# Optimization experiments

Hardware: AMD Instinct MI355X
Metric: run time of the kernel (lower is better)

## Reference

```python
import jax, jax.numpy as jnp
import numpy as np

B, D, H, E = 1024, 64, 128, 8192


def setup_inputs() -> dict:
    key = jax.random.key(0)
    ks = jax.random.split(key, 10)
    def w(k, shape, fan_in):
        return jax.random.normal(k, shape, jnp.float32) / np.float32(np.sqrt(fan_in))
    return {
        "mu": jax.random.normal(ks[0], (B, D), jnp.float32),
        "current_edge_index": jax.random.randint(ks[1], (2, E), 0, B),
        "W1": w(ks[2], (D, H), D),   "b1": jnp.zeros((H,), jnp.float32),
        "W2": w(ks[3], (H, H), H),   "b2": jnp.zeros((H,), jnp.float32),
        "Ws1": w(ks[4], (2 * H, H), 2 * H), "bs1": jnp.zeros((H,), jnp.float32),
        "Ws2": w(ks[5], (H, 1), H),  "bs2": jnp.zeros((1,), jnp.float32),
        "Wg1": w(ks[6], (2 * H, H), 2 * H), "bg1": jnp.zeros((H,), jnp.float32),
        "Wg2": w(ks[7], (H, D), H), "bg2": jnp.zeros((D,), jnp.float32),
    }


def _gcn(x, W, b, src, dst, n):
    loop = jnp.arange(n)
    s = jnp.concatenate([src, loop])
    d = jnp.concatenate([dst, loop])
    deg = jax.ops.segment_sum(jnp.ones_like(s, x.dtype), d, num_segments=n)
    dinv = jax.lax.rsqrt(jnp.maximum(deg, 1e-12))
    norm = dinv[s] * dinv[d]                      # [E+n]
    xw = x @ W                                    # [n,H]
    out = jax.ops.segment_sum(xw[s] * norm[:, None], d, num_segments=n)
    return out + b


def _pairwise_scores(h, Ws1, bs1, Ws2, bs2):
    # score_mlp([h_i || h_j]) for all pairs, vectorized: split first-layer weight
    A = h @ Ws1[:H]                               # [B,H] contribution of h_i
    C = h @ Ws1[H:]                               # [B,H] contribution of h_j
    pre = jax.nn.relu(A[:, None, :] + C[None, :, :] + bs1)   # [B,B,H]
    s = (pre @ Ws2)[..., 0] + bs2[0]              # [B,B]
    up = jnp.triu(s, 1)                           # only i<j computed in original
    return up + up.T                              # symmetric, zero diagonal


def _kruskal(scores_np, n):
    iu, ju = np.triu_indices(n, 1)
    w = scores_np[iu, ju]
    order = np.argsort(-w, kind="stable")         # descending, stable like list.sort
    parent = list(range(n))
    rank = [0] * n
    def find(u):
        while parent[u] != u:
            parent[u] = parent[parent[u]]
            u = parent[u]
        return u
    edges = []
    for k in order:
        i, j = int(iu[k]), int(ju[k])
        ri, rj = find(i), find(j)
        if ri == rj:
            continue
        if rank[ri] < rank[rj]:
            parent[ri] = rj
        elif rank[ri] > rank[rj]:
            parent[rj] = ri
        else:
            parent[rj] = ri
            rank[ri] += 1
        edges.append((i, j))
        if len(edges) == n - 1:
            break
    return np.asarray(edges, dtype=np.int64)      # [n-1, 2]


def reference(mu, current_edge_index, W1, b1, W2, b2, Ws1, bs1, Ws2, bs2, Wg1, bg1, Wg2, bg2):
    src, dst = current_edge_index[0], current_edge_index[1]
    h = jax.nn.relu(_gcn(mu, W1, b1, src, dst, B))
    h = jax.nn.relu(_gcn(h, W2, b2, src, dst, B))
    scores = _pairwise_scores(h, Ws1, bs1, Ws2, bs2)          # [B,B]
    mst = _kruskal(np.asarray(scores), B)                     # [B-1,2], i<j
    ei = jnp.asarray(mst[:, 0])
    ej = jnp.asarray(mst[:, 1])
    # bidirectional edge index: src=[i,j,...], dst=[j,i,...]
    new_edge_index = jnp.stack([
        jnp.stack([ei, ej], axis=1).reshape(-1),
        jnp.stack([ej, ei], axis=1).reshape(-1),
    ], axis=0)                                                # [2, 2*(B-1)]
    hp = jnp.concatenate([h[ei], h[ej]], axis=1)              # [B-1, 2H]
    gamma = jnp.tanh(jax.nn.relu(hp @ Wg1 + bg1) @ Wg2 + bg2) # [B-1, D]
    return (new_edge_index, gamma)
```

## Files before the change

kernel.cpp:

```cpp
#include <hip/hip_runtime.h>
#include <hip/hip_bf16.h>
#include <math.h>

#define BN 1024
#define DIN 64
#define HD 128
#define EN 8192
#define SLOTS_STRIDE 64
#define MMR 8

__global__ void k_init(int* cnt, int* comp, unsigned long long* best, int* mstcnt, int* done_ctr) {
    int i = blockIdx.x * blockDim.x + threadIdx.x;
    if (i < BN) { cnt[i] = 0; comp[i] = i; best[i] = 0ull; }
    if (i < 16) done_ctr[i] = 0;
    if (i == 0) *mstcnt = 0;
}

__global__ void k_fill(const int* dst, int* cnt, int* slots) {
    int e = blockIdx.x * blockDim.x + threadIdx.x;
    if (e < EN) {
        int d = dst[e];
        int p = atomicAdd(&cnt[d], 1);
        if (p < SLOTS_STRIDE) slots[d * SLOTS_STRIDE + p] = e;
    }
}

__global__ __launch_bounds__(128) void k_finish(int* slots, const int* cnt, float* dinv) {
    __shared__ int buf[128][65];
    int tid = threadIdx.x;
    int t = blockIdx.x * 128 + tid;
    int n = cnt[t];
    if (n > SLOTS_STRIDE) n = SLOTS_STRIDE;
    for (int k = 0; k < n; k++) buf[tid][k] = slots[t * SLOTS_STRIDE + k];
    for (int k = 1; k < n; k++) {
        int v = buf[tid][k];
        int q = k - 1;
        while (q >= 0 && buf[tid][q] > v) { buf[tid][q + 1] = buf[tid][q]; q--; }
        buf[tid][q + 1] = v;
    }
    for (int k = 0; k < n; k++) slots[t * SLOTS_STRIDE + k] = buf[tid][k];
    dinv[t] = 1.0f / sqrtf(fmaxf((float)(n + 1), 1e-12f));
}

__global__ __launch_bounds__(128) void k_mm8(const float* x, const float* W, const float* bias,
                                             float* out, int K) {
    __shared__ float xr[MMR][HD];
    int col = threadIdx.x;
    int r0 = blockIdx.x * MMR;
#pragma unroll
    for (int r = 0; r < MMR; r++)
        if (col < K) xr[r][col] = x[(r0 + r) * K + col];
    __syncthreads();
    float b = bias ? bias[col] : 0.0f;
    float acc[MMR];
#pragma unroll
    for (int r = 0; r < MMR; r++) acc[r] = b;
#pragma unroll 4
    for (int k = 0; k < K; k++) {
        float w = W[k * HD + col];
#pragma unroll
        for (int r = 0; r < MMR; r++) acc[r] = fmaf(xr[r][k], w, acc[r]);
    }
#pragma unroll
    for (int r = 0; r < MMR; r++) out[(r0 + r) * HD + col] = acc[r];
}

__global__ __launch_bounds__(128) void k_mmAC(const float* h, const float* Ws1, const float* bs1,
                                              float* Aa, float* Cc) {
    __shared__ float xr[MMR][HD];
    int col = threadIdx.x;
    int r0 = blockIdx.x * MMR;
#pragma unroll
    for (int r = 0; r < MMR; r++) xr[r][col] = h[(r0 + r) * HD + col];
    __syncthreads();
    float accA[MMR], accC[MMR];
    float bc = bs1[col];
#pragma unroll
    for (int r = 0; r < MMR; r++) { accA[r] = 0.0f; accC[r] = bc; }
#pragma unroll 2
    for (int k = 0; k < HD; k++) {
        float wa = Ws1[k * HD + col];
        float wc = Ws1[(HD + k) * HD + col];
#pragma unroll
        for (int r = 0; r < MMR; r++) {
            accA[r] = fmaf(xr[r][k], wa, accA[r]);
            accC[r] = fmaf(xr[r][k], wc, accC[r]);
        }
    }
#pragma unroll
    for (int r = 0; r < MMR; r++) {
        Aa[(r0 + r) * HD + col] = accA[r];
        Cc[(r0 + r) * HD + col] = accC[r];
    }
}

__global__ __launch_bounds__(128) void k_gather(const float* xw, const float* bvec, const int* src,
                                                const int* slots, const int* cnt,
                                                const float* dinv, float* hout) {
    int d = blockIdx.x, t = threadIdx.x;
    float dd = dinv[d];
    float acc = 0.0f;
    int base = d * SLOTS_STRIDE, n = cnt[d];
    if (n > SLOTS_STRIDE) n = SLOTS_STRIDE;
    for (int s = 0; s < n; s++) {
        int e = slots[base + s];
        int sn = src[e];
        acc = fmaf(xw[sn * HD + t], dinv[sn] * dd, acc);
    }
    acc = fmaf(xw[d * HD + t], dd * dd, acc);
    acc += bvec[t];
    hout[d * HD + t] = fmaxf(acc, 0.0f);
}

__global__ __launch_bounds__(256) void k_scores(const float* Aa, const float* Cc,
                                                const float* Ws2, const float* bs2v, float* S) {
    int bi = blockIdx.y, bj = blockIdx.x;
    if (bi > bj) return;
    __shared__ float As[64][68];
    __shared__ float Cs[64][68];
    __shared__ float w2[HD];
    int tid = threadIdx.x;
    int R = bi * 64, Cb = bj * 64;
    if (tid < HD) w2[tid] = Ws2[tid];
    int tx = tid & 15, ty = tid >> 4;
    float acc[4][4] = {};
    for (int half = 0; half < 2; half++) {
        int k0 = half * 64;
        __syncthreads();
        for (int idx = tid; idx < 64 * 64; idx += 256) {
            int row = idx >> 6;
            int kk = idx & 63;
            As[kk][row] = Aa[(R + row) * HD + k0 + kk];
            Cs[kk][row] = Cc[(Cb + row) * HD + k0 + kk];
        }
        __syncthreads();
        for (int kk = 0; kk < 64; kk++) {
            float4 av = *(const float4*)&As[kk][ty * 4];
            float4 cv = *(const float4*)&Cs[kk][tx * 4];
            float wk = w2[k0 + kk];
            float ar[4] = {av.x, av.y, av.z, av.w};
            float cr[4] = {cv.x, cv.y, cv.z, cv.w};
#pragma unroll
            for (int r = 0; r < 4; r++)
#pragma unroll
                for (int q = 0; q < 4; q++) {
                    float tv = fmaxf(ar[r] + cr[q], 0.0f);
                    acc[r][q] = fmaf(tv, wk, acc[r][q]);
                }
        }
    }
    float b2 = bs2v[0];
#pragma unroll
    for (int r = 0; r < 4; r++)
#pragma unroll
        for (int q = 0; q < 4; q++) {
            int gr = R + ty * 4 + r, gc = Cb + tx * 4 + q;
            float v = acc[r][q] + b2;
            if (gr < gc) { S[gr * BN + gc] = v; S[gc * BN + gr] = v; }
            else if (gr == gc) S[gr * BN + gc] = 0.0f;
        }
}

__device__ __forceinline__ unsigned long long edge_key(float w, int i, int j) {
    unsigned u = __float_as_uint(w);
    u = (u & 0x80000000u) ? ~u : (u | 0x80000000u);
    int a = i < j ? i : j, b = i < j ? j : i;
    unsigned packed = (unsigned)(a * BN + b);
    return ((unsigned long long)u << 20) | (unsigned long long)(0xFFFFFu - packed);
}

__global__ __launch_bounds__(256) void k_round(const float* S, int* comp,
                                               unsigned long long* best,
                                               unsigned long long* mst, int* mstcnt,
                                               int* done_ctr, int round) {
    __shared__ unsigned long long red[256];
    __shared__ int pa[BN], pb[BN];
    __shared__ int isLast;
    int tid = threadIdx.x;
    if (*mstcnt >= BN - 1) return;
    int i = blockIdx.x;
    int ci = comp[i];
    unsigned long long loc = 0ull;
    for (int j = tid; j < BN; j += 256) {
        if (comp[j] != ci) {
            unsigned long long key = edge_key(S[i * BN + j], i, j);
            if (key > loc) loc = key;
        }
    }
    red[tid] = loc;
    __syncthreads();
    for (int s = 128; s > 0; s >>= 1) {
        if (tid < s) {
            unsigned long long o = red[tid + s];
            if (o > red[tid]) red[tid] = o;
        }
        __syncthreads();
    }
    if (tid == 0) {
        if (red[0]) atomicMax(&best[ci], red[0]);
        __threadfence();
        int v = atomicAdd(&done_ctr[round], 1);
        isLast = (v == BN - 1) ? 1 : 0;
    }
    __syncthreads();
    if (!isLast) return;
    __threadfence();
    for (int c = tid; c < BN; c += 256) {
        int myComp = comp[c];
        bool root = (myComp == c);
        unsigned long long e = best[c];
        int t = c;
        if (root && e) {
            unsigned packed = 0xFFFFFu - (unsigned)(e & 0xFFFFFu);
            int a = packed >> 10, b = packed & 1023;
            int ca = comp[a], cb = comp[b];
            t = (ca == c) ? cb : ca;
        }
        pa[c] = (root && e) ? t : c;
    }
    __syncthreads();
    for (int c = tid; c < BN; c += 256) {
        int myComp = comp[c];
        bool root = (myComp == c);
        unsigned long long e = best[c];
        int p0 = pa[c];
        if (root && e) {
            int t = pa[c];
            bool mutual = (pa[t] == c);
            if (mutual && c < t) p0 = c;
            if (!(mutual && c > t)) {
                int idx = atomicAdd(mstcnt, 1);
                mst[idx] = e;
            }
        }
        pb[c] = p0;
    }
    __syncthreads();
    for (int c = tid; c < BN; c += 256) pa[c] = pb[c];
    __syncthreads();
    for (int it = 0; it < 10; it++) {
        for (int c = tid; c < BN; c += 256) pb[c] = pa[pa[c]];
        __syncthreads();
        for (int c = tid; c < BN; c += 256) pa[c] = pb[c];
        __syncthreads();
    }
    for (int c = tid; c < BN; c += 256) {
        comp[c] = pa[comp[c]];
        best[c] = 0ull;
    }
}

__global__ __launch_bounds__(1024) void k_sort(const unsigned long long* mst, float* out, int* pairs) {
    __shared__ unsigned long long s[BN];
    int tid = threadIdx.x;
    s[tid] = (tid < BN - 1) ? mst[tid] : 0ull;
    __syncthreads();
    for (int k = 2; k <= BN; k <<= 1)
        for (int j = k >> 1; j > 0; j >>= 1) {
            int l = tid ^ j;
            if (l > tid) {
                unsigned long long x = s[tid], y = s[l];
                bool up = ((tid & k) == 0);
                if ((x > y) == up) { s[tid] = y; s[l] = x; }
            }
            __syncthreads();
        }
    if (tid < BN - 1) {
        unsigned long long key = s[BN - 1 - tid];
        unsigned packed = 0xFFFFFu - (unsigned)(key & 0xFFFFFu);
        int i = packed >> 10, j2 = packed & 1023;
        out[2 * tid] = (float)i;
        out[2 * tid + 1] = (float)j2;
        out[2046 + 2 * tid] = (float)j2;
        out[2046 + 2 * tid + 1] = (float)i;
        pairs[2 * tid] = i;
        pairs[2 * tid + 1] = j2;
    }
}

__global__ __launch_bounds__(128) void k_gamma(const float* h, const int* pairs,
                                               const float* Wg1, const float* bg1,
                                               const float* Wg2, const float* bg2, float* out) {
    int eidx = blockIdx.x;
    __shared__ float hp[2 * HD];
    __shared__ float z1[HD];
    int t = threadIdx.x;
    int i = pairs[2 * eidx], j = pairs[2 * eidx + 1];
    hp[t] = h[i * HD + t];
    hp[HD + t] = h[j * HD + t];
    __syncthreads();
    float acc = bg1[t];
    for (int k = 0; k < 2 * HD; k++) acc = fmaf(hp[k], Wg1[k * HD + t], acc);
    z1[t] = fmaxf(acc, 0.0f);
    __syncthreads();
    if (t < DIN) {
        float g = bg2[t];
        for (int k = 0; k < HD; k++) g = fmaf(z1[k], Wg2[k * DIN + t], g);
        out[4092 + eidx * DIN + t] = tanhf(g);
    }
}

extern "C" void kernel_launch(void* const* d_in, const int* in_sizes, int n_in,
                              void* d_out, int out_size, void* d_ws, size_t ws_size,
                              hipStream_t stream) {
    const float* mu  = (const float*)d_in[0];
    const int*   ei  = (const int*)d_in[1];
    const float* W1  = (const float*)d_in[2];
    const float* b1  = (const float*)d_in[3];
    const float* W2  = (const float*)d_in[4];
    const float* b2  = (const float*)d_in[5];
    const float* Ws1 = (const float*)d_in[6];
    const float* bs1 = (const float*)d_in[7];
    const float* Ws2 = (const float*)d_in[8];
    const float* bs2 = (const float*)d_in[9];
    const float* Wg1 = (const float*)d_in[10];
    const float* bg1 = (const float*)d_in[11];
    const float* Wg2 = (const float*)d_in[12];
    const float* bg2 = (const float*)d_in[13];
    float* out = (float*)d_out;

    const int* src = ei;
    const int* dst = ei + EN;

    char* ws = (char*)d_ws;
    int*   slots = (int*)(ws);
    int*   cnt   = (int*)(ws + 262144);
    float* dinv  = (float*)(ws + 266240);
    float* S     = (float*)(ws);
    float* xw    = (float*)(ws + 4194304);
    float* h1    = (float*)(ws + 4718592);
    float* h2    = (float*)(ws + 5242880);
    float* Aa    = (float*)(ws + 5767168);
    float* Cc    = (float*)(ws + 6291456);
    int*   comp  = (int*)(ws + 6815744);
    unsigned long long* best = (unsigned long long*)(ws + 6819840);
    unsigned long long* mst  = (unsigned long long*)(ws + 6828032);
    int*   mstcnt = (int*)(ws + 6836224);
    int*   pairs  = (int*)(ws + 6840320);
    int*   done_ctr = (int*)(ws + 6848512);

    k_init<<<4, 256, 0, stream>>>(cnt, comp, best, mstcnt, done_ctr);
    k_fill<<<EN / 256, 256, 0, stream>>>(dst, cnt, slots);
    k_finish<<<BN / 128, 128, 0, stream>>>(slots, cnt, dinv);

    k_mm8<<<BN / MMR, HD, 0, stream>>>(mu, W1, nullptr, xw, DIN);
    k_gather<<<BN, HD, 0, stream>>>(xw, b1, src, slots, cnt, dinv, h1);
    k_mm8<<<BN / MMR, HD, 0, stream>>>(h1, W2, nullptr, xw, HD);
    k_gather<<<BN, HD, 0, stream>>>(xw, b2, src, slots, cnt, dinv, h2);

    k_mmAC<<<BN / MMR, HD, 0, stream>>>(h2, Ws1, bs1, Aa, Cc);

    k_scores<<<dim3(16, 16), 256, 0, stream>>>(Aa, Cc, Ws2, bs2, S);

    for (int r = 0; r < 10; r++)
        k_round<<<BN, 256, 0, stream>>>(S, comp, best, mst, mstcnt, done_ctr, r);

    k_sort<<<1, 1024, 0, stream>>>(mst, out, pairs);
    k_gamma<<<BN - 1, HD, 0, stream>>>(h2, pairs, Wg1, bg1, Wg2, bg2, out);
}
```

Measured before the change: 188.2 us.

## Split Boruvka round into per-row best kernel and single-block merge kernel

Replaces the fused Boruvka round, which used a last-block-done atomic counter with threadfences, with two launches per round. The first is a wave-per-row best-edge kernel using shuffle reductions. The second is a 1024-thread single-block merge kernel. The separate bitonic sort kernel is removed: the merge kernel writes the final sorted edges by computing each edge's rank by counting, once the MST is complete. This removes the serialized last-block tail and the block-wide shared reductions, but doubles the number of launches per round and adds an O(n^2) rank count.

```diff
diff --git a/kernel.cpp b/kernel.cpp
--- a/kernel.cpp
+++ b/kernel.cpp
@@ -9,10 +9,11 @@
 #define SLOTS_STRIDE 64
 #define MMR 8
 
-__global__ void k_init(int* cnt, int* comp, unsigned long long* best, int* mstcnt, int* done_ctr) {
+typedef unsigned long long u64;
+
+__global__ void k_init(int* cnt, int* comp, u64* best, int* mstcnt) {
     int i = blockIdx.x * blockDim.x + threadIdx.x;
     if (i < BN) { cnt[i] = 0; comp[i] = i; best[i] = 0ull; }
-    if (i < 16) done_ctr[i] = 0;
     if (i == 0) *mstcnt = 0;
 }
 
@@ -161,120 +162,88 @@
         }
 }
 
-__device__ __forceinline__ unsigned long long edge_key(float w, int i, int j) {
+__device__ __forceinline__ u64 edge_key(float w, int i, int j) {
     unsigned u = __float_as_uint(w);
     u = (u & 0x80000000u) ? ~u : (u | 0x80000000u);
     int a = i < j ? i : j, b = i < j ? j : i;
     unsigned packed = (unsigned)(a * BN + b);
-    return ((unsigned long long)u << 20) | (unsigned long long)(0xFFFFFu - packed);
-}
-
-__global__ __launch_bounds__(256) void k_round(const float* S, int* comp,
-                                               unsigned long long* best,
-                                               unsigned long long* mst, int* mstcnt,
-                                               int* done_ctr, int round) {
-    __shared__ unsigned long long red[256];
+    return ((u64)u << 20) | (u64)(0xFFFFFu - packed);
+}
+
+__global__ __launch_bounds__(256) void k_best(const float* S, const int* comp,
+                                              u64* best, const int* mstcnt) {
+    if (*mstcnt >= BN - 1) return;
+    int lane = threadIdx.x & 63;
+    int i = blockIdx.x * 4 + (threadIdx.x >> 6);
+    int ci = comp[i];
+    const float* Srow = S + (size_t)i * BN;
+    u64 loc = 0ull;
+    for (int j = lane; j < BN; j += 64)
+        if (comp[j] != ci) {
+            u64 key = edge_key(Srow[j], i, j);
+            if (key > loc) loc = key;
+        }
+#pragma unroll
+    for (int off = 32; off > 0; off >>= 1) {
+        u64 o = __shfl_xor(loc, off);
+        if (o > loc) loc = o;
+    }
+    if (lane == 0 && loc) atomicMax(&best[ci], loc);
+}
+
+__global__ __launch_bounds__(1024) void k_merge(int* comp, u64* best, u64* mst, int* mstcnt,
+                                                float* out, int* pairs) {
     __shared__ int pa[BN], pb[BN];
-    __shared__ int isLast;
-    int tid = threadIdx.x;
+    __shared__ u64 sk[BN];
+    int c = threadIdx.x;
     if (*mstcnt >= BN - 1) return;
-    int i = blockIdx.x;
-    int ci = comp[i];
-    unsigned long long loc = 0ull;
-    for (int j = tid; j < BN; j += 256) {
-        if (comp[j] != ci) {
-            unsigned long long key = edge_key(S[i * BN + j], i, j);
-            if (key > loc) loc = key;
-        }
-    }
-    red[tid] = loc;
-    __syncthreads();
-    for (int s = 128; s > 0; s >>= 1) {
-        if (tid < s) {
-            unsigned long long o = red[tid + s];
-            if (o > red[tid]) red[tid] = o;
-        }
-        __syncthreads();
-    }
-    if (tid == 0) {
-        if (red[0]) atomicMax(&best[ci], red[0]);
-        __threadfence();
-        int v = atomicAdd(&done_ctr[round], 1);
-        isLast = (v == BN - 1) ? 1 : 0;
-    }
-    __syncthreads();
-    if (!isLast) return;
-    __threadfence();
-    for (int c = tid; c < BN; c += 256) {
-        int myComp = comp[c];
-        bool root = (myComp == c);
-        unsigned long long e = best[c];
-        int t = c;
-        if (root && e) {
-            unsigned packed = 0xFFFFFu - (unsigned)(e & 0xFFFFFu);
-            int a = packed >> 10, b = packed & 1023;
-            int ca = comp[a], cb = comp[b];
-            t = (ca == c) ? cb : ca;
-        }
-        pa[c] = (root && e) ? t : c;
-    }
-    __syncthreads();
-    for (int c = tid; c < BN; c += 256) {
-        int myComp = comp[c];
-        bool root = (myComp == c);
-        unsigned long long e = best[c];
-        int p0 = pa[c];
-        if (root && e) {
-            int t = pa[c];
-            bool mutual = (pa[t] == c);
-            if (mutual && c < t) p0 = c;
-            if (!(mutual && c > t)) {
-                int idx = atomicAdd(mstcnt, 1);
-                mst[idx] = e;
-            }
-        }
-        pb[c] = p0;
-    }
-    __syncthreads();
-    for (int c = tid; c < BN; c += 256) pa[c] = pb[c];
-    __syncthreads();
+    int myComp = comp[c];
+    bool root = (myComp == c);
+    u64 e = best[c];
+    int t = c;
+    if (root && e) {
+        unsigned packed = 0xFFFFFu - (unsigned)(e & 0xFFFFFu);
+        int a = packed >> 10, b = packed & 1023;
+        int ca = comp[a], cb = comp[b];
+        t = (ca == c) ? cb : ca;
+    }
+    pa[c] = (root && e) ? t : c;
+    __syncthreads();
+    bool mutual = root && e && (pa[t] == c);
+    int p0 = pa[c];
+    if (mutual && c < t) p0 = c;
+    __syncthreads();
+    pa[c] = p0;
+    __syncthreads();
+    if (root && e && !(mutual && c > t)) {
+        int idx = atomicAdd(mstcnt, 1);
+        mst[idx] = e;
+    }
     for (int it = 0; it < 10; it++) {
-        for (int c = tid; c < BN; c += 256) pb[c] = pa[pa[c]];
-        __syncthreads();
-        for (int c = tid; c < BN; c += 256) pa[c] = pb[c];
-        __syncthreads();
-    }
-    for (int c = tid; c < BN; c += 256) {
-        comp[c] = pa[comp[c]];
-        best[c] = 0ull;
-    }
-}
-
-__global__ __launch_bounds__(1024) void k_sort(const unsigned long long* mst, float* out, int* pairs) {
-    __shared__ unsigned long long s[BN];
-    int tid = threadIdx.x;
-    s[tid] = (tid < BN - 1) ? mst[tid] : 0ull;
-    __syncthreads();
-    for (int k = 2; k <= BN; k <<= 1)
-        for (int j = k >> 1; j > 0; j >>= 1) {
-            int l = tid ^ j;
-            if (l > tid) {
-                unsigned long long x = s[tid], y = s[l];
-                bool up = ((tid & k) == 0);
-                if ((x > y) == up) { s[tid] = y; s[l] = x; }
-            }
-            __syncthreads();
-        }
-    if (tid < BN - 1) {
-        unsigned long long key = s[BN - 1 - tid];
-        unsigned packed = 0xFFFFFu - (unsigned)(key & 0xFFFFFu);
-        int i = packed >> 10, j2 = packed & 1023;
-        out[2 * tid] = (float)i;
-        out[2 * tid + 1] = (float)j2;
-        out[2046 + 2 * tid] = (float)j2;
-        out[2046 + 2 * tid + 1] = (float)i;
-        pairs[2 * tid] = i;
-        pairs[2 * tid + 1] = j2;
+        pb[c] = pa[pa[c]];
+        __syncthreads();
+        pa[c] = pb[c];
+        __syncthreads();
+    }
+    comp[c] = pa[myComp];
+    best[c] = 0ull;
+    __syncthreads();
+    if (*mstcnt == BN - 1) {
+        sk[c] = (c < BN - 1) ? mst[c] : 0ull;
+        __syncthreads();
+        if (c < BN - 1) {
+            u64 mykey = sk[c];
+            int rk = 0;
+            for (int f = 0; f < BN - 1; f++) rk += (sk[f] > mykey) ? 1 : 0;
+            unsigned packed = 0xFFFFFu - (unsigned)(mykey & 0xFFFFFu);
+            int i = packed >> 10, j2 = packed & 1023;
+            out[2 * rk] = (float)i;
+            out[2 * rk + 1] = (float)j2;
+            out[2046 + 2 * rk] = (float)j2;
+            out[2046 + 2 * rk + 1] = (float)i;
+            pairs[2 * rk] = i;
+            pairs[2 * rk + 1] = j2;
+        }
     }
 }
 
@@ -333,13 +302,12 @@
     float* Aa    = (float*)(ws + 5767168);
     float* Cc    = (float*)(ws + 6291456);
     int*   comp  = (int*)(ws + 6815744);
-    unsigned long long* best = (unsigned long long*)(ws + 6819840);
-    unsigned long long* mst  = (unsigned long long*)(ws + 6828032);
+    u64*   best  = (u64*)(ws + 6819840);
+    u64*   mst   = (u64*)(ws + 6828032);
     int*   mstcnt = (int*)(ws + 6836224);
     int*   pairs  = (int*)(ws + 6840320);
-    int*   done_ctr = (int*)(ws + 6848512);
-
-    k_init<<<4, 256, 0, stream>>>(cnt, comp, best, mstcnt, done_ctr);
+
+    k_init<<<4, 256, 0, stream>>>(cnt, comp, best, mstcnt);
     k_fill<<<EN / 256, 256, 0, stream>>>(dst, cnt, slots);
     k_finish<<<BN / 128, 128, 0, stream>>>(slots, cnt, dinv);
 
@@ -352,9 +320,10 @@
 
     k_scores<<<dim3(16, 16), 256, 0, stream>>>(Aa, Cc, Ws2, bs2, S);
 
-    for (int r = 0; r < 10; r++)
-        k_round<<<BN, 256, 0, stream>>>(S, comp, best, mst, mstcnt, done_ctr, r);
-
-    k_sort<<<1, 1024, 0, stream>>>(mst, out, pairs);
+    for (int r = 0; r < 10; r++) {
+        k_best<<<BN / 4, 256, 0, stream>>>(S, comp, best, mstcnt);
+        k_merge<<<1, 1024, 0, stream>>>(comp, best, mst, mstcnt, out, pairs);
+    }
+
     k_gamma<<<BN - 1, HD, 0, stream>>>(h2, pairs, Wg1, bg1, Wg2, bg2, out);
 }
```

After: 190.2 us. No clear change (+1.1%).
